# Kernel tuning notes

Hardware: AMD Instinct MI355X
Metric: run time of the kernel (lower is better)

## Reference

```python
import jax, jax.numpy as jnp
import numpy as np

N, T, DF, H, NH, E = 512, 60, 6, 64, 2, 8192
NEG = -1e10

def _leaky(x):
    return jnp.where(x >= 0, x, 0.01 * x)

def _ln(x, g, b, eps=1e-5):
    m = x.mean(-1, keepdims=True)
    v = ((x - m) ** 2).mean(-1, keepdims=True)
    return (x - m) / jnp.sqrt(v + eps) * g + b

def _gru_layer(xs, wih, whh, bih, bhh):
    # xs: (N, T, H_in) -> (N, T, H); torch GRU gate math
    h0 = jnp.zeros((xs.shape[0], whh.shape[1]), xs.dtype)
    def step(h, xt):
        gi = xt @ wih.T + bih
        gh = h @ whh.T + bhh
        ir, iz, inn = jnp.split(gi, 3, -1)
        hr, hz, hn = jnp.split(gh, 3, -1)
        r = jax.nn.sigmoid(ir + hr)
        z = jax.nn.sigmoid(iz + hz)
        n = jnp.tanh(inn + r * hn)
        h = (1 - z) * n + z * h
        return h, h
    _, hs = jax.lax.scan(step, h0, jnp.swapaxes(xs, 0, 1))
    return jnp.swapaxes(hs, 0, 1)

def _forward(x, edge_index, fc_in_w, fc_in_b, gru_wih0, gru_whh0, gru_bih0, gru_bhh0, gru_wih1, gru_whh1, gru_bih1, gru_bhh1, dm_qw, dm_kw, dm_vw, dm_vb, ssa_qw, ssa_kw, ssa_vw, ssa_vb, ln1_g, ln1_b, ln2_g, ln2_b, mlp_w1, mlp_b1, mlp_w2, mlp_b2, mha_in_w, mha_in_b, mha_out_w, mha_out_b, gf_xs_w, gf_xt_w, gf_xt_b, gf_h_w, gf_h_b, lin_w, lin_b):
    h = x @ fc_in_w.T + fc_in_b                      # (N, T, H)
    # temporal encoder: 2-layer GRU + leaky relu
    g = _gru_layer(h, gru_wih0, gru_whh0, gru_bih0, gru_bhh0)
    g = _gru_layer(g, gru_wih1, gru_whh1, gru_bih1, gru_bhh1)
    ts = _leaky(g)
    res_ts = ts[:, -1, :]                            # (N, H)
    # spatial sparse transformer: time T acts as batch, attention over stocks N
    xs = jnp.swapaxes(h, 0, 1)                       # (T, N, H)
    hd = H // NH
    q = (xs @ dm_qw.T).reshape(T, N, NH, hd).transpose(0, 2, 1, 3)
    k = (xs @ dm_kw.T).reshape(T, N, NH, hd).transpose(0, 2, 1, 3)
    v = (xs @ dm_vw.T + dm_vb).reshape(T, N, NH, hd).transpose(0, 2, 1, 3)
    attn = jnp.einsum('thnd,thmd->thnm', q, k) * (H ** -0.5)  # scale uses full dim C, as in source
    dmask = attn >= attn.mean(-1, keepdims=True)     # dynamic per-row mean threshold
    attn_s = jax.nn.softmax(jnp.where(dmask, attn, NEG), axis=-1)
    dyn = jnp.einsum('thnm,thmd->thnd', attn_s, v).transpose(0, 2, 1, 3).reshape(T, N, H)
    # SSA: static graph mask from edge_index
    qs = xs @ ssa_qw.T
    ks2 = xs @ ssa_kw.T
    vs = xs @ ssa_vw.T + ssa_vb
    a2 = jnp.einsum('tnc,tmc->tnm', qs, ks2) * (H ** -0.5)
    adj = jnp.zeros((N, N), jnp.float32).at[edge_index[0], edge_index[1]].add(1.0)
    gmask = adj >= 1.0
    a2s = jax.nn.softmax(jnp.where(gmask[None, :, :], a2, NEG), axis=-1)
    stat = jnp.einsum('tnm,tmc->tnc', a2s, vs)
    residual = dyn + stat + xs
    o = _ln(residual, ln1_g, ln1_b)
    o = (o @ mlp_w1.T + mlp_b1) @ mlp_w2.T + mlp_b2  # two linears, no activation (as in source)
    o = _ln(o + residual, ln2_g, ln2_b)
    move = _leaky(o)                                 # (T, N, H)
    # spatial embedding aggregation: sinusoidal PE + 1-head MHA over time
    pos = jnp.arange(T, dtype=jnp.float32)[:, None]
    div = jnp.exp(jnp.arange(0, H, 2, dtype=jnp.float32) * (-np.log(10000.0) / H))
    pe = jnp.zeros((T, H), jnp.float32).at[:, 0::2].set(jnp.sin(pos * div)).at[:, 1::2].set(jnp.cos(pos * div))
    src = move + pe[:, None, :]
    mq, mk, mv = jnp.split(src @ mha_in_w.T + mha_in_b, 3, axis=-1)
    sc = jnp.einsum('tnh,snh->nts', mq, mk) * (H ** -0.5)
    mo = jnp.einsum('nts,snh->tnh', jax.nn.softmax(sc, -1), mv) @ mha_out_w.T + mha_out_b
    agg = mo[-1]                                     # (N, H)
    mu = agg.mean(-1, keepdims=True)
    var = ((agg - mu) ** 2).mean(-1, keepdims=True)
    agg = (agg - mu) / jnp.sqrt(var + 1e-5)          # param-free layer_norm
    # gated fusion
    zg = jax.nn.sigmoid(agg @ gf_xs_w.T + res_ts @ gf_xt_w.T + gf_xt_b)
    fused = _leaky((zg * agg + (1 - zg) * res_ts) @ gf_h_w.T + gf_h_b)
    out = (fused @ lin_w.T + lin_b)[:, 0]
    return out, attn_s

def setup_inputs() -> dict:
    key = jax.random.key(0)
    ks = jax.random.split(key, 40)
    def w(i, shape):
        return jax.random.normal(ks[i], shape, jnp.float32) * 0.05
    return {
        'x': jax.random.normal(ks[0], (N, T, DF), jnp.float32),
        'edge_index': jax.random.randint(ks[1], (2, E), 0, N),
        'fc_in_w': w(2, (H, DF)), 'fc_in_b': w(3, (H,)),
        'gru_wih0': w(4, (3 * H, H)), 'gru_whh0': w(5, (3 * H, H)), 'gru_bih0': w(6, (3 * H,)), 'gru_bhh0': w(7, (3 * H,)),
        'gru_wih1': w(8, (3 * H, H)), 'gru_whh1': w(9, (3 * H, H)), 'gru_bih1': w(10, (3 * H,)), 'gru_bhh1': w(11, (3 * H,)),
        'dm_qw': w(12, (H, H)), 'dm_kw': w(13, (H, H)), 'dm_vw': w(14, (H, H)), 'dm_vb': w(15, (H,)),
        'ssa_qw': w(16, (H, H)), 'ssa_kw': w(17, (H, H)), 'ssa_vw': w(18, (H, H)), 'ssa_vb': w(19, (H,)),
        'ln1_g': jnp.ones((H,), jnp.float32), 'ln1_b': jnp.zeros((H,), jnp.float32),
        'ln2_g': jnp.ones((H,), jnp.float32), 'ln2_b': jnp.zeros((H,), jnp.float32),
        'mlp_w1': w(20, (2 * H, H)), 'mlp_b1': w(21, (2 * H,)), 'mlp_w2': w(22, (H, 2 * H)), 'mlp_b2': w(23, (H,)),
        'mha_in_w': w(24, (3 * H, H)), 'mha_in_b': w(25, (3 * H,)), 'mha_out_w': w(26, (H, H)), 'mha_out_b': w(27, (H,)),
        'gf_xs_w': w(28, (H, H)), 'gf_xt_w': w(29, (H, H)), 'gf_xt_b': w(30, (H,)),
        'gf_h_w': w(31, (H, H)), 'gf_h_b': w(32, (H,)),
        'lin_w': w(33, (1, H)), 'lin_b': w(34, (1,)),
    }

def reference(x, edge_index, fc_in_w, fc_in_b, gru_wih0, gru_whh0, gru_bih0, gru_bhh0, gru_wih1, gru_whh1, gru_bih1, gru_bhh1, dm_qw, dm_kw, dm_vw, dm_vb, ssa_qw, ssa_kw, ssa_vw, ssa_vb, ln1_g, ln1_b, ln2_g, ln2_b, mlp_w1, mlp_b1, mlp_w2, mlp_b2, mha_in_w, mha_in_b, mha_out_w, mha_out_b, gf_xs_w, gf_xt_w, gf_xt_b, gf_h_w, gf_h_b, lin_w, lin_b):
    return _forward(x, edge_index, fc_in_w, fc_in_b, gru_wih0, gru_whh0, gru_bih0, gru_bhh0, gru_wih1, gru_whh1, gru_bih1, gru_bhh1, dm_qw, dm_kw, dm_vw, dm_vb, ssa_qw, ssa_kw, ssa_vw, ssa_vb, ln1_g, ln1_b, ln2_g, ln2_b, mlp_w1, mlp_b1, mlp_w2, mlp_b2, mha_in_w, mha_in_b, mha_out_w, mha_out_b, gf_xs_w, gf_xt_w, gf_xt_b, gf_h_w, gf_h_b, lin_w, lin_b)
```

## Files before the change

kernel.cpp:

```cpp
#include <hip/hip_runtime.h>
#include <hip/hip_bf16.h>

#define NN 512
#define TT 60
#define DFF 6
#define EE 8192
#define TN (TT*NN)
#define TCH 20
#define NCHK 3
#define SCALEV 0.125f
#define NEGV -1.0e10f

typedef __hip_bfloat16 bf16;
using bfrag8 = __attribute__((ext_vector_type(8))) short;
using facc4  = __attribute__((ext_vector_type(4))) float;

__device__ __forceinline__ float b2f(bf16 v){ return __bfloat162float(v); }
__device__ __forceinline__ bf16 f2b(float v){ return __float2bfloat16(v); }
__device__ __forceinline__ float lk(float x){ return x >= 0.f ? x : 0.01f*x; }
__device__ __forceinline__ float sgm(float x){ return 1.f/(1.f+__expf(-x)); }

__device__ __forceinline__ float ldf(const float* p, long i){ return p[i]; }
__device__ __forceinline__ float ldf(const bf16* p, long i){ return b2f(p[i]); }
__device__ __forceinline__ void stf(float* p, long i, float v){ p[i] = v; }
__device__ __forceinline__ void stf(bf16* p, long i, float v){ p[i] = f2b(v); }

__device__ __forceinline__ float4 ld4f(const float* p){ return *(const float4*)p; }
__device__ __forceinline__ float4 ld4f(const bf16* p){
  ushort4 u = *(const ushort4*)p;
  float4 f;
  f.x = b2f(*(const bf16*)&u.x);
  f.y = b2f(*(const bf16*)&u.y);
  f.z = b2f(*(const bf16*)&u.z);
  f.w = b2f(*(const bf16*)&u.w);
  return f;
}

__device__ __forceinline__ float wsum64(float v){
  #pragma unroll
  for (int off = 32; off; off >>= 1) v += __shfl_xor(v, off, 64);
  return v;
}
__device__ __forceinline__ float wmax64(float v){
  #pragma unroll
  for (int off = 32; off; off >>= 1) v = fmaxf(v, __shfl_xor(v, off, 64));
  return v;
}

__global__ __launch_bounds__(256) void k_zero_u32(unsigned int* __restrict__ p, int n){
  int i = blockIdx.x*256 + threadIdx.x;
  if (i < n) p[i] = 0u;
}
__global__ __launch_bounds__(256) void k_scatter_bits(const int* __restrict__ ei, unsigned int* __restrict__ msk){
  int e = blockIdx.x*256 + threadIdx.x;
  if (e < EE) {
    int u = ei[e], v = ei[EE + e];
    atomicOr(&msk[u*16 + (v >> 5)], 1u << (v & 31));
  }
}

__global__ __launch_bounds__(256) void k_pack(
  const float* __restrict__ qw, const float* __restrict__ kw,
  const float* __restrict__ qsw, const float* __restrict__ ksw,
  const float* __restrict__ vw, const float* __restrict__ vsw,
  const float* __restrict__ vb, const float* __restrict__ vsb,
  float* __restrict__ Wall, float* __restrict__ bcV)
{
  int idx = blockIdx.x*256 + threadIdx.x;
  if (idx < 6*4096) {
    int which = idx >> 12, rem = idx & 4095;
    const float* s = (which==0)?qw:(which==1)?kw:(which==2)?qsw:(which==3)?ksw:(which==4)?vw:vsw;
    Wall[idx] = s[rem];
  } else if (idx < 6*4096 + 128) {
    int o = idx - 6*4096;
    bcV[o] = (o < 64) ? vb[o] : vsb[o-64];
  }
}

__global__ __launch_bounds__(256) void k_fcin(
  const float* __restrict__ x, const float* __restrict__ w, const float* __restrict__ b,
  float* __restrict__ xs, float* __restrict__ resid)
{
  long idx = (long)blockIdx.x*256 + threadIdx.x;
  int o = idx & 63;
  long r = idx >> 6;
  int t = (int)(r / NN), n = (int)(r % NN);
  const float* xr = x + ((long)n*TT + t)*DFF;
  const float* wr = w + o*DFF;
  float acc = 0.f;
  #pragma unroll
  for (int j = 0; j < DFF; ++j) acc = fmaf(xr[j], wr[j], acc);
  float h = __fadd_rn(acc, b[o]);
  xs[idx] = h;
  resid[idx] = h;
}

__global__ __launch_bounds__(256) void k_proj(
  const float* __restrict__ A, const float* __restrict__ Wall, const float* __restrict__ bcV,
  float* __restrict__ qkx, float* __restrict__ qkc, bf16* __restrict__ vvc)
{
  __shared__ float As[64][68];
  __shared__ float Bs[64][68];
  int rt = blockIdx.x, bcn = blockIdx.y;
  const float* B = Wall + bcn*4096;
  int tid = threadIdx.x;
  int tx = tid & 15, ty = tid >> 4;
  float acc[4][4] = {{0.f}};
  #pragma unroll
  for (int i = 0; i < 4; ++i) {
    int t = i*256 + tid;
    int m = t >> 4, kq = (t & 15)*4;
    float4 av = *(const float4*)&A[(long)(rt*64 + m)*64 + kq];
    As[kq+0][m] = av.x; As[kq+1][m] = av.y; As[kq+2][m] = av.z; As[kq+3][m] = av.w;
    float4 bv = *(const float4*)&B[(long)m*64 + kq];
    Bs[kq+0][m] = bv.x; Bs[kq+1][m] = bv.y; Bs[kq+2][m] = bv.z; Bs[kq+3][m] = bv.w;
  }
  __syncthreads();
  for (int kk = 0; kk < 64; ++kk) {
    float4 a4 = *(const float4*)&As[kk][ty*4];
    float4 b4 = *(const float4*)&Bs[kk][tx*4];
    acc[0][0] = fmaf(a4.x,b4.x,acc[0][0]); acc[0][1] = fmaf(a4.x,b4.y,acc[0][1]); acc[0][2] = fmaf(a4.x,b4.z,acc[0][2]); acc[0][3] = fmaf(a4.x,b4.w,acc[0][3]);
    acc[1][0] = fmaf(a4.y,b4.x,acc[1][0]); acc[1][1] = fmaf(a4.y,b4.y,acc[1][1]); acc[1][2] = fmaf(a4.y,b4.z,acc[1][2]); acc[1][3] = fmaf(a4.y,b4.w,acc[1][3]);
    acc[2][0] = fmaf(a4.z,b4.x,acc[2][0]); acc[2][1] = fmaf(a4.z,b4.y,acc[2][1]); acc[2][2] = fmaf(a4.z,b4.z,acc[2][2]); acc[2][3] = fmaf(a4.z,b4.w,acc[2][3]);
    acc[3][0] = fmaf(a4.w,b4.x,acc[3][0]); acc[3][1] = fmaf(a4.w,b4.y,acc[3][1]); acc[3][2] = fmaf(a4.w,b4.z,acc[3][2]); acc[3][3] = fmaf(a4.w,b4.w,acc[3][3]);
  }
  if (bcn < 4) {
    float* C = (bcn < 2) ? qkx : qkc;
    int cb = (bcn & 1)*64;
    #pragma unroll
    for (int i = 0; i < 4; ++i) {
      long ro = (long)(rt*64 + ty*4 + i)*128 + cb + tx*4;
      #pragma unroll
      for (int j = 0; j < 4; ++j) C[ro + j] = acc[i][j];
    }
  } else {
    int cb = (bcn - 4)*64;
    float bv[4];
    #pragma unroll
    for (int j = 0; j < 4; ++j) bv[j] = bcV[cb + tx*4 + j];
    #pragma unroll
    for (int i = 0; i < 4; ++i) {
      long ro = (long)(rt*64 + ty*4 + i)*128 + cb + tx*4;
      #pragma unroll
      for (int j = 0; j < 4; ++j) vvc[ro + j] = f2b(acc[i][j] + bv[j]);
    }
  }
}

template<typename TA, typename TC>
__global__ __launch_bounds__(256) void k_gemm(
  const TA* __restrict__ A, const float* __restrict__ B, const float* __restrict__ bias,
  TC* __restrict__ C, int KD, int NC, int gather)
{
  __shared__ float As[64][68];
  __shared__ float Bs[64][68];
  int rt = blockIdx.x, bcn = blockIdx.y;
  int tid = threadIdx.x;
  int tx = tid & 15, ty = tid >> 4;
  float acc[4][4] = {{0.f}};
  int nch = KD >> 6;
  for (int kc = 0; kc < nch; ++kc) {
    __syncthreads();
    #pragma unroll
    for (int i = 0; i < 4; ++i) {
      int t = i*256 + tid;
      int m = t >> 4, kq = (t & 15)*4;
      long aoff;
      int r = rt*64 + m;
      if (gather) { int n2 = r / TT, t2 = r - n2*TT; aoff = ((long)t2*NN + n2)*64 + kc*64 + kq; }
      else aoff = (long)r*KD + kc*64 + kq;
      float4 av = ld4f(A + aoff);
      As[kq+0][m] = av.x; As[kq+1][m] = av.y; As[kq+2][m] = av.z; As[kq+3][m] = av.w;
      int col = bcn*64 + m;
      float4 bv = *(const float4*)&B[(long)col*KD + kc*64 + kq];
      Bs[kq+0][m] = bv.x; Bs[kq+1][m] = bv.y; Bs[kq+2][m] = bv.z; Bs[kq+3][m] = bv.w;
    }
    __syncthreads();
    #pragma unroll 8
    for (int kk = 0; kk < 64; ++kk) {
      float4 a4 = *(const float4*)&As[kk][ty*4];
      float4 b4 = *(const float4*)&Bs[kk][tx*4];
      acc[0][0] += a4.x*b4.x; acc[0][1] += a4.x*b4.y; acc[0][2] += a4.x*b4.z; acc[0][3] += a4.x*b4.w;
      acc[1][0] += a4.y*b4.x; acc[1][1] += a4.y*b4.y; acc[1][2] += a4.y*b4.z; acc[1][3] += a4.y*b4.w;
      acc[2][0] += a4.z*b4.x; acc[2][1] += a4.z*b4.y; acc[2][2] += a4.z*b4.z; acc[2][3] += a4.z*b4.w;
      acc[3][0] += a4.w*b4.x; acc[3][1] += a4.w*b4.y; acc[3][2] += a4.w*b4.z; acc[3][3] += a4.w*b4.w;
    }
  }
  float bv[4];
  #pragma unroll
  for (int j = 0; j < 4; ++j) bv[j] = bias ? bias[bcn*64 + tx*4 + j] : 0.f;
  #pragma unroll
  for (int i = 0; i < 4; ++i) {
    long ro = (long)(rt*64 + ty*4 + i)*NC + bcn*64 + tx*4;
    #pragma unroll
    for (int j = 0; j < 4; ++j) stf(C, ro + j, acc[i][j] + bv[j]);
  }
}

__global__ __launch_bounds__(192) void k_gru(
  const float* __restrict__ gi, const float* __restrict__ whh, const float* __restrict__ bhh,
  bf16* __restrict__ g_out, float* __restrict__ res_out, int layer)
{
  int n = blockIdx.x;
  int tid = threadIdx.x;
  int g = tid >> 6, o = tid & 63;
  __shared__ __align__(16) float h_lds[64];
  __shared__ float ghs[3][64];
  float4 w4[16];
  #pragma unroll
  for (int k4 = 0; k4 < 16; ++k4)
    w4[k4] = *(const float4*)&whh[(long)(g*64+o)*64 + k4*4];
  float bh = bhh[g*64+o];
  if (tid < 64) h_lds[tid] = 0.f;
  __syncthreads();
  const float4* h4 = (const float4*)h_lds;
  for (int t = 0; t < TT; ++t) {
    float p0 = 0.f, p1 = 0.f, p2 = 0.f, p3 = 0.f;
    #pragma unroll
    for (int k4 = 0; k4 < 16; ++k4) {
      float4 hv = h4[k4];
      p0 = fmaf(w4[k4].x, hv.x, p0);
      p1 = fmaf(w4[k4].y, hv.y, p1);
      p2 = fmaf(w4[k4].z, hv.z, p2);
      p3 = fmaf(w4[k4].w, hv.w, p3);
    }
    ghs[g][o] = bh + ((p0 + p1) + (p2 + p3));
    __syncthreads();
    if (tid < 64) {
      const float* gib = gi + ((long)n*TT + t)*192;
      float ir = gib[o], iz = gib[64+o], inn = gib[128+o];
      float r = sgm(ir + ghs[0][o]);
      float z = sgm(iz + ghs[1][o]);
      float nn2 = tanhf(inn + r*ghs[2][o]);
      float hn = (1.f - z)*nn2 + z*h_lds[o];
      h_lds[o] = hn;
      if (layer == 0) g_out[((long)t*NN + n)*64 + o] = f2b(hn);
      else if (t == TT-1) res_out[(long)n*64 + o] = lk(hn);
    }
    __syncthreads();
  }
}

#define MULADD4(QV, KV) \
  v0 = __fadd_rn(v0, __fmul_rn((QV).x, (KV).x)); \
  v1 = __fadd_rn(v1, __fmul_rn((QV).y, (KV).y)); \
  v2 = __fadd_rn(v2, __fmul_rn((QV).z, (KV).z)); \
  v3 = __fadd_rn(v3, __fmul_rn((QV).w, (KV).w));

__global__ __launch_bounds__(256, 3) void k_attn_dyn(
  const float* __restrict__ qkx, const bf16* __restrict__ vvc,
  float* __restrict__ attn_out, float* __restrict__ resid, int tc)
{
  __shared__ __align__(16) char smem[52288];
  float* sc    = (float*)smem;
  bf16*  vT    = (bf16*)smem;
  float* kt    = (float*)(smem + 33280);
  bf16*  p_lds = (bf16*)(smem + 33280);
  float* red   = (float*)(smem + 49920);
  float* ulds  = (float*)(smem + 51712);
  float* means = (float*)(smem + 52224);

  int qt = blockIdx.x, h = blockIdx.y, lt = blockIdx.z;
  int gt = tc*TCH + lt;
  int tid = threadIdx.x, tx = tid & 31, grp = tid >> 5;
  int qbase = grp*2;
  int qce = h*32, kce = 64 + h*32;

  float4 q0r[8], q1r[8];
  {
    const float* qp = qkx + ((long)(lt*NN + qt*16 + qbase))*128 + qce;
    #pragma unroll
    for (int j = 0; j < 8; ++j) q0r[j] = *(const float4*)(qp + j*4);
    #pragma unroll
    for (int j = 0; j < 8; ++j) q1r[j] = *(const float4*)(qp + 128 + j*4);
  }

  float S[2][16];
  for (int p = 0; p < 4; ++p) {
    __syncthreads();
    for (int i = tid; i < 1024; i += 256) {
      int row = i >> 3, jj = (i & 7) << 2;
      *(float4*)(kt + row*36 + jj) =
        *(const float4*)(qkx + ((long)(lt*NN + p*128 + row))*128 + kce + jj);
    }
    __syncthreads();
    #pragma unroll
    for (int ii = 0; ii < 4; ++ii) {
      int m = tx + 32*ii;
      const float4* kr4 = (const float4*)(kt + m*36);
      float4 k0 = kr4[0], k1 = kr4[1], k2 = kr4[2], k3 = kr4[3];
      float4 k4 = kr4[4], k5 = kr4[5], k6 = kr4[6], k7 = kr4[7];
      {
        float v0 = 0.f, v1 = 0.f, v2 = 0.f, v3 = 0.f;
        MULADD4(q0r[0], k0); MULADD4(q0r[1], k1); MULADD4(q0r[2], k2); MULADD4(q0r[3], k3);
        MULADD4(q0r[4], k4); MULADD4(q0r[5], k5); MULADD4(q0r[6], k6); MULADD4(q0r[7], k7);
        float s = __fadd_rn(__fadd_rn(v0, v1), __fadd_rn(v2, v3));
        s = s * 0.125f;
        S[0][p*4+ii] = s;
        sc[(qbase+0)*520 + p*128 + m] = s;
      }
      {
        float v0 = 0.f, v1 = 0.f, v2 = 0.f, v3 = 0.f;
        MULADD4(q1r[0], k0); MULADD4(q1r[1], k1); MULADD4(q1r[2], k2); MULADD4(q1r[3], k3);
        MULADD4(q1r[4], k4); MULADD4(q1r[5], k5); MULADD4(q1r[6], k6); MULADD4(q1r[7], k7);
        float s = __fadd_rn(__fadd_rn(v0, v1), __fadd_rn(v2, v3));
        s = s * 0.125f;
        S[1][p*4+ii] = s;
        sc[(qbase+1)*520 + p*128 + m] = s;
      }
    }
  }
  __syncthreads();
  if (tid < 128) {
    int row = tid >> 3, b = (tid >> 1) & 3, hh = tid & 1;
    const float* a = sc + row*520 + b*128 + hh*4;
    float4 r4 = *(const float4*)a;
    #pragma unroll
    for (int i = 8; i < 128; i += 8) {
      float4 v = *(const float4*)(a + i);
      r4.x = __fadd_rn(r4.x, v.x); r4.y = __fadd_rn(r4.y, v.y);
      r4.z = __fadd_rn(r4.z, v.z); r4.w = __fadd_rn(r4.w, v.w);
    }
    ulds[row*8 + b*2 + hh] = __fadd_rn(__fadd_rn(r4.x, r4.y), __fadd_rn(r4.z, r4.w));
  }
  __syncthreads();
  if (tid < 16) {
    const float* ur = ulds + tid*8;
    float p0 = __fadd_rn(ur[0], ur[1]);
    float p1 = __fadd_rn(ur[2], ur[3]);
    float p2 = __fadd_rn(ur[4], ur[5]);
    float p3 = __fadd_rn(ur[6], ur[7]);
    means[tid] = __fadd_rn(__fadd_rn(p0, p1), __fadd_rn(p2, p3)) * (1.f/512.f);
  }
  __syncthreads();

  long obase = ((long)(gt*2 + h))*NN*NN;
  #pragma unroll
  for (int qi = 0; qi < 2; ++qi) {
    float mn = means[qbase + qi];
    unsigned kmask = 0; float lm = -INFINITY;
    #pragma unroll
    for (int ig = 0; ig < 16; ++ig) {
      if (S[qi][ig] >= mn) { kmask |= (1u << ig); lm = fmaxf(lm, S[qi][ig]); }
    }
    #pragma unroll
    for (int mk = 1; mk < 32; mk <<= 1) lm = fmaxf(lm, __shfl_xor(lm, mk, 64));
    float e[16]; float se = 0.f;
    #pragma unroll
    for (int ig = 0; ig < 16; ++ig) {
      e[ig] = ((kmask >> ig) & 1u) ? __expf(S[qi][ig] - lm) : 0.f;
      se += e[ig];
    }
    #pragma unroll
    for (int mk = 1; mk < 32; mk <<= 1) se += __shfl_xor(se, mk, 64);
    float inv = 1.f/se;
    float* rowp = attn_out + obase + (long)(qt*16 + qbase + qi)*NN;
    bf16* prow = p_lds + (qbase + qi)*520;
    #pragma unroll
    for (int ig = 0; ig < 16; ++ig) {
      float pr = e[ig]*inv;
      rowp[tx + 32*ig] = pr;
      prow[tx + 32*ig] = f2b(pr);
    }
  }

  for (int i = tid; i < 2048; i += 256) {
    int m2 = (i & 255) << 1;
    int cc = (i >> 8) << 2;
    const bf16* gp = vvc + ((long)(lt*NN + m2))*128 + qce + cc;
    ushort4 a = *(const ushort4*)(gp);
    ushort4 b = *(const ushort4*)(gp + 128);
    *(unsigned*)(vT + (cc+0)*520 + m2) = (unsigned)a.x | ((unsigned)b.x << 16);
    *(unsigned*)(vT + (cc+1)*520 + m2) = (unsigned)a.y | ((unsigned)b.y << 16);
    *(unsigned*)(vT + (cc+2)*520 + m2) = (unsigned)a.z | ((unsigned)b.z << 16);
    *(unsigned*)(vT + (cc+3)*520 + m2) = (unsigned)a.w | ((unsigned)b.w << 16);
  }
  __syncthreads();

  {
    int w = tid >> 6, l = tid & 63;
    int nh = w & 1, kh = w >> 1;
    int arow = l & 15, kgrp = l >> 4;
    facc4 acc = {0.f, 0.f, 0.f, 0.f};
    const bf16* pa = p_lds + arow*520 + kh*256 + kgrp*8;
    const bf16* pb = vT + (nh*16 + arow)*520 + kh*256 + kgrp*8;
    #pragma unroll
    for (int ks = 0; ks < 8; ++ks) {
      bfrag8 av = *(const bfrag8*)(pa + ks*32);
      bfrag8 bv = *(const bfrag8*)(pb + ks*32);
      acc = __builtin_amdgcn_mfma_f32_16x16x32_bf16(av, bv, acc, 0, 0, 0);
    }
    if (w >= 2) {
      #pragma unroll
      for (int r = 0; r < 4; ++r)
        red[nh*272 + (kgrp*4 + r)*17 + arow] = acc[r];
    }
    __syncthreads();
    if (w < 2) {
      long rb = ((long)gt*NN + qt*16)*64 + h*32 + nh*16 + arow;
      #pragma unroll
      for (int r = 0; r < 4; ++r) {
        int row = kgrp*4 + r;
        resid[rb + (long)row*64] += acc[r] + red[nh*272 + row*17 + arow];
      }
    }
  }
}

__global__ __launch_bounds__(256, 3) void k_attn_st(
  const float* __restrict__ qkc, const bf16* __restrict__ vvc,
  const unsigned int* __restrict__ msk, float* __restrict__ resid, int tc)
{
  __shared__ __align__(16) char smem[51456];
  float* kc  = (float*)smem;
  bf16*  vTh = (bf16*)smem;
  float* qtl = (float*)(smem + 34816);
  bf16*  P   = (bf16*)(smem + 34816);

  int qt = blockIdx.x, lt = blockIdx.z;
  int gt = tc*TCH + lt;
  int tid = threadIdx.x;
  int tx = tid & 31, grp = tid >> 5;
  int qbase = grp*2;

  float4* q4 = (float4*)qtl;
  float4* k4 = (float4*)kc;

  {
    int m = tid >> 4, jc = tid & 15;
    q4[m*17 + jc] = *(const float4*)(qkc + ((long)(lt*NN + qt*16 + m))*128 + jc*4);
  }

  float S[2][16];
  for (int p = 0; p < 4; ++p) {
    __syncthreads();
    for (int i = tid; i < 2048; i += 256) {
      int m = i >> 4, jc = i & 15;
      k4[m*17 + (jc ^ ((m >> 2) & 3))] =
        *(const float4*)(qkc + ((long)(lt*NN + p*128 + m))*128 + 64 + jc*4);
    }
    __syncthreads();
    float acc00 = 0.f, acc01 = 0.f, acc02 = 0.f, acc03 = 0.f;
    float acc10 = 0.f, acc11 = 0.f, acc12 = 0.f, acc13 = 0.f;
    #pragma unroll 4
    for (int jc = 0; jc < 16; ++jc) {
      float4 q0 = q4[(qbase+0)*17 + jc];
      float4 q1 = q4[(qbase+1)*17 + jc];
      float4 kv;
      int m0 = tx;
      kv = k4[m0*17 + (jc ^ ((m0 >> 2) & 3))];
      acc00 += q0.x*kv.x + q0.y*kv.y + q0.z*kv.z + q0.w*kv.w;
      acc10 += q1.x*kv.x + q1.y*kv.y + q1.z*kv.z + q1.w*kv.w;
      int m1 = tx + 32;
      kv = k4[m1*17 + (jc ^ ((m1 >> 2) & 3))];
      acc01 += q0.x*kv.x + q0.y*kv.y + q0.z*kv.z + q0.w*kv.w;
      acc11 += q1.x*kv.x + q1.y*kv.y + q1.z*kv.z + q1.w*kv.w;
      int m2 = tx + 64;
      kv = k4[m2*17 + (jc ^ ((m2 >> 2) & 3))];
      acc02 += q0.x*kv.x + q0.y*kv.y + q0.z*kv.z + q0.w*kv.w;
      acc12 += q1.x*kv.x + q1.y*kv.y + q1.z*kv.z + q1.w*kv.w;
      int m3 = tx + 96;
      kv = k4[m3*17 + (jc ^ ((m3 >> 2) & 3))];
      acc03 += q0.x*kv.x + q0.y*kv.y + q0.z*kv.z + q0.w*kv.w;
      acc13 += q1.x*kv.x + q1.y*kv.y + q1.z*kv.z + q1.w*kv.w;
    }
    S[0][p*4+0] = acc00; S[0][p*4+1] = acc01; S[0][p*4+2] = acc02; S[0][p*4+3] = acc03;
    S[1][p*4+0] = acc10; S[1][p*4+1] = acc11; S[1][p*4+2] = acc12; S[1][p*4+3] = acc13;
  }
  __syncthreads();

  #pragma unroll
  for (int qi = 0; qi < 2; ++qi) {
    #pragma unroll
    for (int ig = 0; ig < 16; ++ig) S[qi][ig] *= SCALEV;
    float lm = -INFINITY;
    #pragma unroll
    for (int ig = 0; ig < 16; ++ig) {
      bool keep = ((msk[(qt*16 + qbase + qi)*16 + ig] >> tx) & 1u) != 0u;
      float v = keep ? S[qi][ig] : NEGV;
      S[qi][ig] = v;
      lm = fmaxf(lm, v);
    }
    #pragma unroll
    for (int mk = 1; mk < 32; mk <<= 1) lm = fmaxf(lm, __shfl_xor(lm, mk, 64));
    float se = 0.f;
    #pragma unroll
    for (int ig = 0; ig < 16; ++ig) {
      float ev = __expf(S[qi][ig] - lm);
      S[qi][ig] = ev;
      se += ev;
    }
    #pragma unroll
    for (int mk = 1; mk < 32; mk <<= 1) se += __shfl_xor(se, mk, 64);
    float inv = 1.f / se;
    bf16* prow = P + (qbase + qi)*520;
    #pragma unroll
    for (int ig = 0; ig < 16; ++ig)
      prow[tx + 32*ig] = f2b(S[qi][ig]*inv);
  }

  int w = tid >> 6, l = tid & 63;
  int arow = l & 15, kgrp = l >> 4;
  facc4 acc = {0.f, 0.f, 0.f, 0.f};
  for (int kh = 0; kh < 2; ++kh) {
    __syncthreads();
    for (int i = tid; i < 2048; i += 256) {
      int m2 = (i & 127) << 1;
      int cc = (i >> 7) << 2;
      const bf16* gp = vvc + ((long)(lt*NN + kh*256 + m2))*128 + 64 + cc;
      ushort4 a = *(const ushort4*)(gp);
      ushort4 b = *(const ushort4*)(gp + 128);
      *(unsigned*)(vTh + (cc+0)*264 + m2) = (unsigned)a.x | ((unsigned)b.x << 16);
      *(unsigned*)(vTh + (cc+1)*264 + m2) = (unsigned)a.y | ((unsigned)b.y << 16);
      *(unsigned*)(vTh + (cc+2)*264 + m2) = (unsigned)a.z | ((unsigned)b.z << 16);
      *(unsigned*)(vTh + (cc+3)*264 + m2) = (unsigned)a.w | ((unsigned)b.w << 16);
    }
    __syncthreads();
    const bf16* pa = P + arow*520 + kh*256 + kgrp*8;
    const bf16* pb = vTh + (w*16 + arow)*264 + kgrp*8;
    #pragma unroll
    for (int ks = 0; ks < 8; ++ks) {
      bfrag8 av = *(const bfrag8*)(pa + ks*32);
      bfrag8 bv = *(const bfrag8*)(pb + ks*32);
      acc = __builtin_amdgcn_mfma_f32_16x16x32_bf16(av, bv, acc, 0, 0, 0);
    }
  }
  long rb = ((long)gt*NN + qt*16)*64 + w*16 + arow;
  #pragma unroll
  for (int r = 0; r < 4; ++r) {
    int row = kgrp*4 + r;
    resid[rb + (long)row*64] += acc[r];
  }
}

__global__ __launch_bounds__(256) void k_ln1(
  const float* __restrict__ resid, const float* __restrict__ gw, const float* __restrict__ bw,
  float* __restrict__ ln1o)
{
  int lane = threadIdx.x & 63;
  long r = (long)blockIdx.x*4 + (threadIdx.x >> 6);
  long base = r*64 + lane;
  float v = resid[base];
  float m = wsum64(v)*(1.f/64.f);
  float d = v - m;
  float var = wsum64(d*d)*(1.f/64.f);
  ln1o[base] = d*rsqrtf(var + 1e-5f)*gw[lane] + bw[lane];
}

__global__ __launch_bounds__(256) void k_ln2_src(
  const float* __restrict__ mlpo, const float* __restrict__ resid,
  const float* __restrict__ gw, const float* __restrict__ bw,
  float* __restrict__ src)
{
  int lane = threadIdx.x & 63;
  long r = (long)blockIdx.x*4 + (threadIdx.x >> 6);
  long base = r*64 + lane;
  float v = mlpo[base] + resid[base];
  float m = wsum64(v)*(1.f/64.f);
  float d = v - m;
  float var = wsum64(d*d)*(1.f/64.f);
  float y = d*rsqrtf(var + 1e-5f)*gw[lane] + bw[lane];
  y = lk(y);
  float tf = (float)(r / NN);
  float dv = __expf(-(float)(lane & ~1) * 0.14391156831212787f);
  float pe = (lane & 1) ? cosf(tf*dv) : sinf(tf*dv);
  src[base] = y + pe;
}

__global__ __launch_bounds__(64) void k_head(
  const bf16* __restrict__ mqkv, const float* __restrict__ rts,
  const float* __restrict__ mow, const float* __restrict__ mob,
  const float* __restrict__ xsw, const float* __restrict__ xtw, const float* __restrict__ xtb,
  const float* __restrict__ hw, const float* __restrict__ hb,
  const float* __restrict__ linw, const float* __restrict__ linb,
  float* __restrict__ out)
{
  int n = blockIdx.x, o = threadIdx.x;
  __shared__ float ps[TT];
  __shared__ float buf[64], buf2[64];
  float mq = b2f(mqkv[((long)(TT-1)*NN + n)*192 + o]);
  for (int s = 0; s < TT; ++s) {
    float v = mq * b2f(mqkv[((long)s*NN + n)*192 + 64 + o]);
    v = wsum64(v);
    if (o == 0) ps[s] = v * SCALEV;
  }
  __syncthreads();
  float x = (o < TT) ? ps[o] : -INFINITY;
  float mx = wmax64(x);
  float e = (o < TT) ? __expf(x - mx) : 0.f;
  float se = wsum64(e);
  if (o < TT) ps[o] = e / se;
  __syncthreads();
  float acc = 0.f;
  for (int s = 0; s < TT; ++s) acc += ps[s]*b2f(mqkv[((long)s*NN + n)*192 + 128 + o]);
  buf[o] = acc;
  __syncthreads();
  float acc2 = mob[o];
  for (int k = 0; k < 64; ++k) acc2 += buf[k]*mow[o*64 + k];
  float m2 = wsum64(acc2)*(1.f/64.f);
  float d2 = acc2 - m2;
  float var2 = wsum64(d2*d2)*(1.f/64.f);
  float a = d2*rsqrtf(var2 + 1e-5f);
  float rt = rts[(long)n*64 + o];
  __syncthreads();
  buf[o] = a; buf2[o] = rt;
  __syncthreads();
  float pre = xtb[o];
  for (int k = 0; k < 64; ++k) pre += buf[k]*xsw[o*64 + k] + buf2[k]*xtw[o*64 + k];
  float zg = sgm(pre);
  float u = zg*a + (1.f - zg)*rt;
  __syncthreads();
  buf[o] = u;
  __syncthreads();
  float f = hb[o];
  for (int k = 0; k < 64; ++k) f += buf[k]*hw[o*64 + k];
  f = lk(f);
  float tot = wsum64(f * linw[o]);
  if (o == 0) out[n] = tot + linb[0];
}

extern "C" void kernel_launch(void* const* d_in, const int* in_sizes, int n_in,
                              void* d_out, int out_size, void* d_ws, size_t ws_size,
                              hipStream_t stream)
{
  const float* x    = (const float*)d_in[0];
  const int*   ei   = (const int*)  d_in[1];
  const float* fcw  = (const float*)d_in[2];
  const float* fcb  = (const float*)d_in[3];
  const float* wih0 = (const float*)d_in[4];
  const float* whh0 = (const float*)d_in[5];
  const float* bih0 = (const float*)d_in[6];
  const float* bhh0 = (const float*)d_in[7];
  const float* wih1 = (const float*)d_in[8];
  const float* whh1 = (const float*)d_in[9];
  const float* bih1 = (const float*)d_in[10];
  const float* bhh1 = (const float*)d_in[11];
  const float* dmqw = (const float*)d_in[12];
  const float* dmkw = (const float*)d_in[13];
  const float* dmvw = (const float*)d_in[14];
  const float* dmvb = (const float*)d_in[15];
  const float* ssqw = (const float*)d_in[16];
  const float* sskw = (const float*)d_in[17];
  const float* ssvw = (const float*)d_in[18];
  const float* ssvb = (const float*)d_in[19];
  const float* ln1g = (const float*)d_in[20];
  const float* ln1b = (const float*)d_in[21];
  const float* ln2g = (const float*)d_in[22];
  const float* ln2b = (const float*)d_in[23];
  const float* mw1  = (const float*)d_in[24];
  const float* mb1  = (const float*)d_in[25];
  const float* mw2  = (const float*)d_in[26];
  const float* mb2  = (const float*)d_in[27];
  const float* mhw  = (const float*)d_in[28];
  const float* mhb  = (const float*)d_in[29];
  const float* mow  = (const float*)d_in[30];
  const float* mob  = (const float*)d_in[31];
  const float* gxsw = (const float*)d_in[32];
  const float* gxtw = (const float*)d_in[33];
  const float* gxtb = (const float*)d_in[34];
  const float* ghw  = (const float*)d_in[35];
  const float* ghb  = (const float*)d_in[36];
  const float* linw = (const float*)d_in[37];
  const float* linb = (const float*)d_in[38];

  char* base = (char*)d_ws;
  float*  xs    = (float*)(base);
  char*   Rb    = base + 7864320;
  float*  qkc   = (float*)Rb;
  bf16*   vvc   = (bf16*)(Rb + 5242880);
  float*  qkx   = (float*)(Rb + 7864320);
  float*  mlph  = (float*)Rb;
  bf16*   mqkv  = (bf16*)Rb;
  bf16*   g0    = (bf16*)(base + 23592960);
  float*  resid = (float*)(base + 27525120);
  float*  ln1o  = (float*)(base + 35389440);
  float*  rts   = (float*)(base + 43253760);
  unsigned int* msk = (unsigned int*)(base + 43384832);
  float*  Wall  = (float*)(base + 43417600);
  float*  bcV   = (float*)(base + 43515904);
  float*  mlpo  = xs;
  float*  src   = ln1o;
  float*  outb  = (float*)d_out;
  float*  attn  = outb + 512;
  float*  gi    = (float*)((char*)d_out + 2048);

  k_zero_u32<<<dim3(32), 256, 0, stream>>>(msk, 512*16);
  k_scatter_bits<<<dim3(32), 256, 0, stream>>>(ei, msk);
  k_pack<<<dim3(97), 256, 0, stream>>>(dmqw, dmkw, ssqw, sskw, dmvw, ssvw, dmvb, ssvb, Wall, bcV);
  k_fcin<<<dim3(TN*64/256), 256, 0, stream>>>(x, fcw, fcb, xs, resid);
  k_gemm<float,float><<<dim3(480, 3), 256, 0, stream>>>(xs, wih0, bih0, gi, 64, 192, 1);
  k_gru<<<dim3(NN), 192, 0, stream>>>(gi, whh0, bhh0, g0, nullptr, 0);
  k_gemm<bf16,float><<<dim3(480, 3), 256, 0, stream>>>(g0, wih1, bih1, gi, 64, 192, 1);
  k_gru<<<dim3(NN), 192, 0, stream>>>(gi, whh1, bhh1, nullptr, rts, 1);
  for (int tc = 0; tc < NCHK; ++tc) {
    const float* xsc = xs + (size_t)tc*TCH*NN*64;
    k_proj<<<dim3(TCH*NN/64, 6), 256, 0, stream>>>(xsc, Wall, bcV, qkx, qkc, vvc);
    k_attn_dyn<<<dim3(32, 2, TCH), 256, 0, stream>>>(qkx, vvc, attn, resid, tc);
    k_attn_st <<<dim3(32, 1, TCH), 256, 0, stream>>>(qkc, vvc, msk, resid, tc);
  }
  k_ln1<<<dim3(TN/4), 256, 0, stream>>>(resid, ln1g, ln1b, ln1o);
  k_gemm<float,float><<<dim3(480, 2), 256, 0, stream>>>(ln1o, mw1, mb1, mlph, 64, 128, 0);
  k_gemm<float,float><<<dim3(480, 1), 256, 0, stream>>>(mlph, mw2, mb2, mlpo, 128, 64, 0);
  k_ln2_src<<<dim3(TN/4), 256, 0, stream>>>(mlpo, resid, ln2g, ln2b, src);
  k_gemm<float,bf16 ><<<dim3(480, 3), 256, 0, stream>>>(src, mhw, mhb, mqkv, 64, 192, 0);
  k_head<<<dim3(NN), 64, 0, stream>>>(mqkv, rts, mow, mob, gxsw, gxtw, gxtb, ghw, ghb, linw, linb, outb);
}
```

Before: 734.3 us.

## Fuse mask build, attention kernels, and layernorms into neighbouring kernels

Builds the edge bitmask in shared memory inside an extra block of k_pack, replacing the zero and scatter launches. Merges the dynamic and static attention kernels into one launch, with blockIdx.y==2 taking the static path. Folds LN1 into the first MLP GEMM and LN2 plus leaky-ReLU plus positional encoding into the MHA input projection, which removes the intermediate ln1o/src buffers and several launches. In exchange the layernorms are recomputed once per output column tile. The dynamic and static attention blocks now do unsynchronised read-modify-write on the same resid elements in one launch, a possible data race.

```diff
diff --git a/kernel.cpp b/kernel.cpp
--- a/kernel.cpp
+++ b/kernel.cpp
@@ -47,26 +47,28 @@
   return v;
 }
 
-__global__ __launch_bounds__(256) void k_zero_u32(unsigned int* __restrict__ p, int n){
-  int i = blockIdx.x*256 + threadIdx.x;
-  if (i < n) p[i] = 0u;
-}
-__global__ __launch_bounds__(256) void k_scatter_bits(const int* __restrict__ ei, unsigned int* __restrict__ msk){
-  int e = blockIdx.x*256 + threadIdx.x;
-  if (e < EE) {
-    int u = ei[e], v = ei[EE + e];
-    atomicOr(&msk[u*16 + (v >> 5)], 1u << (v & 31));
-  }
-}
-
 __global__ __launch_bounds__(256) void k_pack(
   const float* __restrict__ qw, const float* __restrict__ kw,
   const float* __restrict__ qsw, const float* __restrict__ ksw,
   const float* __restrict__ vw, const float* __restrict__ vsw,
   const float* __restrict__ vb, const float* __restrict__ vsb,
+  const int* __restrict__ ei, unsigned int* __restrict__ msk,
   float* __restrict__ Wall, float* __restrict__ bcV)
 {
-  int idx = blockIdx.x*256 + threadIdx.x;
+  __shared__ unsigned int lmsk[8192];
+  int tid = threadIdx.x;
+  if (blockIdx.x == 97) {
+    for (int i = tid; i < 8192; i += 256) lmsk[i] = 0u;
+    __syncthreads();
+    for (int e = tid; e < EE; e += 256) {
+      int u = ei[e], v = ei[EE + e];
+      atomicOr(&lmsk[u*16 + (v >> 5)], 1u << (v & 31));
+    }
+    __syncthreads();
+    for (int i = tid; i < 8192; i += 256) msk[i] = lmsk[i];
+    return;
+  }
+  int idx = blockIdx.x*256 + tid;
   if (idx < 6*4096) {
     int which = idx >> 12, rem = idx & 4095;
     const float* s = (which==0)?qw:(which==1)?kw:(which==2)?qsw:(which==3)?ksw:(which==4)?vw:vsw;
@@ -247,11 +249,134 @@
   v2 = __fadd_rn(v2, __fmul_rn((QV).z, (KV).z)); \
   v3 = __fadd_rn(v3, __fmul_rn((QV).w, (KV).w));
 
-__global__ __launch_bounds__(256, 3) void k_attn_dyn(
-  const float* __restrict__ qkx, const bf16* __restrict__ vvc,
+__global__ __launch_bounds__(256, 3) void k_attn(
+  const float* __restrict__ qkx, const float* __restrict__ qkc,
+  const bf16* __restrict__ vvc, const unsigned int* __restrict__ msk,
   float* __restrict__ attn_out, float* __restrict__ resid, int tc)
 {
   __shared__ __align__(16) char smem[52288];
+  int qt = blockIdx.x, lt = blockIdx.z;
+  int gt = tc*TCH + lt;
+  int tid = threadIdx.x, tx = tid & 31, grp = tid >> 5;
+  int qbase = grp*2;
+
+  if (blockIdx.y == 2) {
+    float* kc  = (float*)smem;
+    bf16*  vTh = (bf16*)smem;
+    float* qtl = (float*)(smem + 34816);
+    bf16*  P   = (bf16*)(smem + 34816);
+
+    float4* q4 = (float4*)qtl;
+    float4* k4 = (float4*)kc;
+
+    {
+      int m = tid >> 4, jc = tid & 15;
+      q4[m*17 + jc] = *(const float4*)(qkc + ((long)(lt*NN + qt*16 + m))*128 + jc*4);
+    }
+
+    float S[2][16];
+    for (int p = 0; p < 4; ++p) {
+      __syncthreads();
+      for (int i = tid; i < 2048; i += 256) {
+        int m = i >> 4, jc = i & 15;
+        k4[m*17 + (jc ^ ((m >> 2) & 3))] =
+          *(const float4*)(qkc + ((long)(lt*NN + p*128 + m))*128 + 64 + jc*4);
+      }
+      __syncthreads();
+      float acc00 = 0.f, acc01 = 0.f, acc02 = 0.f, acc03 = 0.f;
+      float acc10 = 0.f, acc11 = 0.f, acc12 = 0.f, acc13 = 0.f;
+      #pragma unroll 4
+      for (int jc = 0; jc < 16; ++jc) {
+        float4 q0 = q4[(qbase+0)*17 + jc];
+        float4 q1 = q4[(qbase+1)*17 + jc];
+        float4 kv;
+        int m0 = tx;
+        kv = k4[m0*17 + (jc ^ ((m0 >> 2) & 3))];
+        acc00 += q0.x*kv.x + q0.y*kv.y + q0.z*kv.z + q0.w*kv.w;
+        acc10 += q1.x*kv.x + q1.y*kv.y + q1.z*kv.z + q1.w*kv.w;
+        int m1 = tx + 32;
+        kv = k4[m1*17 + (jc ^ ((m1 >> 2) & 3))];
+        acc01 += q0.x*kv.x + q0.y*kv.y + q0.z*kv.z + q0.w*kv.w;
+        acc11 += q1.x*kv.x + q1.y*kv.y + q1.z*kv.z + q1.w*kv.w;
+        int m2 = tx + 64;
+        kv = k4[m2*17 + (jc ^ ((m2 >> 2) & 3))];
+        acc02 += q0.x*kv.x + q0.y*kv.y + q0.z*kv.z + q0.w*kv.w;
+        acc12 += q1.x*kv.x + q1.y*kv.y + q1.z*kv.z + q1.w*kv.w;
+        int m3 = tx + 96;
+        kv = k4[m3*17 + (jc ^ ((m3 >> 2) & 3))];
+        acc03 += q0.x*kv.x + q0.y*kv.y + q0.z*kv.z + q0.w*kv.w;
+        acc13 += q1.x*kv.x + q1.y*kv.y + q1.z*kv.z + q1.w*kv.w;
+      }
+      S[0][p*4+0] = acc00; S[0][p*4+1] = acc01; S[0][p*4+2] = acc02; S[0][p*4+3] = acc03;
+      S[1][p*4+0] = acc10; S[1][p*4+1] = acc11; S[1][p*4+2] = acc12; S[1][p*4+3] = acc13;
+    }
+    __syncthreads();
+
+    #pragma unroll
+    for (int qi = 0; qi < 2; ++qi) {
+      #pragma unroll
+      for (int ig = 0; ig < 16; ++ig) S[qi][ig] *= SCALEV;
+      float lm = -INFINITY;
+      #pragma unroll
+      for (int ig = 0; ig < 16; ++ig) {
+        bool keep = ((msk[(qt*16 + qbase + qi)*16 + ig] >> tx) & 1u) != 0u;
+        float v = keep ? S[qi][ig] : NEGV;
+        S[qi][ig] = v;
+        lm = fmaxf(lm, v);
+      }
+      #pragma unroll
+      for (int mk = 1; mk < 32; mk <<= 1) lm = fmaxf(lm, __shfl_xor(lm, mk, 64));
+      float se = 0.f;
+      #pragma unroll
+      for (int ig = 0; ig < 16; ++ig) {
+        float ev = __expf(S[qi][ig] - lm);
+        S[qi][ig] = ev;
+        se += ev;
+      }
+      #pragma unroll
+      for (int mk = 1; mk < 32; mk <<= 1) se += __shfl_xor(se, mk, 64);
+      float inv = 1.f / se;
+      bf16* prow = P + (qbase + qi)*520;
+      #pragma unroll
+      for (int ig = 0; ig < 16; ++ig)
+        prow[tx + 32*ig] = f2b(S[qi][ig]*inv);
+    }
+
+    int w = tid >> 6, l = tid & 63;
+    int arow = l & 15, kgrp = l >> 4;
+    facc4 acc = {0.f, 0.f, 0.f, 0.f};
+    for (int kh = 0; kh < 2; ++kh) {
+      __syncthreads();
+      for (int i = tid; i < 2048; i += 256) {
+        int m2 = (i & 127) << 1;
+        int cc = (i >> 7) << 2;
+        const bf16* gp = vvc + ((long)(lt*NN + kh*256 + m2))*128 + 64 + cc;
+        ushort4 a = *(const ushort4*)(gp);
+        ushort4 b = *(const ushort4*)(gp + 128);
+        *(unsigned*)(vTh + (cc+0)*264 + m2) = (unsigned)a.x | ((unsigned)b.x << 16);
+        *(unsigned*)(vTh + (cc+1)*264 + m2) = (unsigned)a.y | ((unsigned)b.y << 16);
+        *(unsigned*)(vTh + (cc+2)*264 + m2) = (unsigned)a.z | ((unsigned)b.z << 16);
+        *(unsigned*)(vTh + (cc+3)*264 + m2) = (unsigned)a.w | ((unsigned)b.w << 16);
+      }
+      __syncthreads();
+      const bf16* pa = P + arow*520 + kh*256 + kgrp*8;
+      const bf16* pb = vTh + (w*16 + arow)*264 + kgrp*8;
+      #pragma unroll
+      for (int ks = 0; ks < 8; ++ks) {
+        bfrag8 av = *(const bfrag8*)(pa + ks*32);
+        bfrag8 bv = *(const bfrag8*)(pb + ks*32);
+        acc = __builtin_amdgcn_mfma_f32_16x16x32_bf16(av, bv, acc, 0, 0, 0);
+      }
+    }
+    long rb = ((long)gt*NN + qt*16)*64 + w*16 + arow;
+    #pragma unroll
+    for (int r = 0; r < 4; ++r) {
+      int row = kgrp*4 + r;
+      resid[rb + (long)row*64] += acc[r];
+    }
+    return;
+  }
+
   float* sc    = (float*)smem;
   bf16*  vT    = (bf16*)smem;
   float* kt    = (float*)(smem + 33280);
@@ -260,10 +385,7 @@
   float* ulds  = (float*)(smem + 51712);
   float* means = (float*)(smem + 52224);
 
-  int qt = blockIdx.x, h = blockIdx.y, lt = blockIdx.z;
-  int gt = tc*TCH + lt;
-  int tid = threadIdx.x, tx = tid & 31, grp = tid >> 5;
-  int qbase = grp*2;
+  int h = blockIdx.y;
   int qce = h*32, kce = 64 + h*32;
 
   float4 q0r[8], q1r[8];
@@ -407,164 +529,97 @@
   }
 }
 
-__global__ __launch_bounds__(256, 3) void k_attn_st(
-  const float* __restrict__ qkc, const bf16* __restrict__ vvc,
-  const unsigned int* __restrict__ msk, float* __restrict__ resid, int tc)
-{
-  __shared__ __align__(16) char smem[51456];
-  float* kc  = (float*)smem;
-  bf16*  vTh = (bf16*)smem;
-  float* qtl = (float*)(smem + 34816);
-  bf16*  P   = (bf16*)(smem + 34816);
-
-  int qt = blockIdx.x, lt = blockIdx.z;
-  int gt = tc*TCH + lt;
+__global__ __launch_bounds__(256) void k_mlp1(
+  const float* __restrict__ resid, const float* __restrict__ g1, const float* __restrict__ b1,
+  const float* __restrict__ B, const float* __restrict__ bias, float* __restrict__ C)
+{
+  __shared__ float As[64][68];
+  __shared__ float Bs[64][68];
+  int rt = blockIdx.x, bcn = blockIdx.y;
   int tid = threadIdx.x;
-  int tx = tid & 31, grp = tid >> 5;
-  int qbase = grp*2;
-
-  float4* q4 = (float4*)qtl;
-  float4* k4 = (float4*)kc;
-
-  {
-    int m = tid >> 4, jc = tid & 15;
-    q4[m*17 + jc] = *(const float4*)(qkc + ((long)(lt*NN + qt*16 + m))*128 + jc*4);
-  }
-
-  float S[2][16];
-  for (int p = 0; p < 4; ++p) {
-    __syncthreads();
-    for (int i = tid; i < 2048; i += 256) {
-      int m = i >> 4, jc = i & 15;
-      k4[m*17 + (jc ^ ((m >> 2) & 3))] =
-        *(const float4*)(qkc + ((long)(lt*NN + p*128 + m))*128 + 64 + jc*4);
-    }
-    __syncthreads();
-    float acc00 = 0.f, acc01 = 0.f, acc02 = 0.f, acc03 = 0.f;
-    float acc10 = 0.f, acc11 = 0.f, acc12 = 0.f, acc13 = 0.f;
-    #pragma unroll 4
-    for (int jc = 0; jc < 16; ++jc) {
-      float4 q0 = q4[(qbase+0)*17 + jc];
-      float4 q1 = q4[(qbase+1)*17 + jc];
-      float4 kv;
-      int m0 = tx;
-      kv = k4[m0*17 + (jc ^ ((m0 >> 2) & 3))];
-      acc00 += q0.x*kv.x + q0.y*kv.y + q0.z*kv.z + q0.w*kv.w;
-      acc10 += q1.x*kv.x + q1.y*kv.y + q1.z*kv.z + q1.w*kv.w;
-      int m1 = tx + 32;
-      kv = k4[m1*17 + (jc ^ ((m1 >> 2) & 3))];
-      acc01 += q0.x*kv.x + q0.y*kv.y + q0.z*kv.z + q0.w*kv.w;
-      acc11 += q1.x*kv.x + q1.y*kv.y + q1.z*kv.z + q1.w*kv.w;
-      int m2 = tx + 64;
-      kv = k4[m2*17 + (jc ^ ((m2 >> 2) & 3))];
-      acc02 += q0.x*kv.x + q0.y*kv.y + q0.z*kv.z + q0.w*kv.w;
-      acc12 += q1.x*kv.x + q1.y*kv.y + q1.z*kv.z + q1.w*kv.w;
-      int m3 = tx + 96;
-      kv = k4[m3*17 + (jc ^ ((m3 >> 2) & 3))];
-      acc03 += q0.x*kv.x + q0.y*kv.y + q0.z*kv.z + q0.w*kv.w;
-      acc13 += q1.x*kv.x + q1.y*kv.y + q1.z*kv.z + q1.w*kv.w;
-    }
-    S[0][p*4+0] = acc00; S[0][p*4+1] = acc01; S[0][p*4+2] = acc02; S[0][p*4+3] = acc03;
-    S[1][p*4+0] = acc10; S[1][p*4+1] = acc11; S[1][p*4+2] = acc12; S[1][p*4+3] = acc13;
-  }
-  __syncthreads();
-
-  #pragma unroll
-  for (int qi = 0; qi < 2; ++qi) {
-    #pragma unroll
-    for (int ig = 0; ig < 16; ++ig) S[qi][ig] *= SCALEV;
-    float lm = -INFINITY;
-    #pragma unroll
-    for (int ig = 0; ig < 16; ++ig) {
-      bool keep = ((msk[(qt*16 + qbase + qi)*16 + ig] >> tx) & 1u) != 0u;
-      float v = keep ? S[qi][ig] : NEGV;
-      S[qi][ig] = v;
-      lm = fmaxf(lm, v);
-    }
-    #pragma unroll
-    for (int mk = 1; mk < 32; mk <<= 1) lm = fmaxf(lm, __shfl_xor(lm, mk, 64));
-    float se = 0.f;
-    #pragma unroll
-    for (int ig = 0; ig < 16; ++ig) {
-      float ev = __expf(S[qi][ig] - lm);
-      S[qi][ig] = ev;
-      se += ev;
-    }
-    #pragma unroll
-    for (int mk = 1; mk < 32; mk <<= 1) se += __shfl_xor(se, mk, 64);
-    float inv = 1.f / se;
-    bf16* prow = P + (qbase + qi)*520;
-    #pragma unroll
-    for (int ig = 0; ig < 16; ++ig)
-      prow[tx + 32*ig] = f2b(S[qi][ig]*inv);
-  }
-
-  int w = tid >> 6, l = tid & 63;
-  int arow = l & 15, kgrp = l >> 4;
-  facc4 acc = {0.f, 0.f, 0.f, 0.f};
-  for (int kh = 0; kh < 2; ++kh) {
-    __syncthreads();
-    for (int i = tid; i < 2048; i += 256) {
-      int m2 = (i & 127) << 1;
-      int cc = (i >> 7) << 2;
-      const bf16* gp = vvc + ((long)(lt*NN + kh*256 + m2))*128 + 64 + cc;
-      ushort4 a = *(const ushort4*)(gp);
-      ushort4 b = *(const ushort4*)(gp + 128);
-      *(unsigned*)(vTh + (cc+0)*264 + m2) = (unsigned)a.x | ((unsigned)b.x << 16);
-      *(unsigned*)(vTh + (cc+1)*264 + m2) = (unsigned)a.y | ((unsigned)b.y << 16);
-      *(unsigned*)(vTh + (cc+2)*264 + m2) = (unsigned)a.z | ((unsigned)b.z << 16);
-      *(unsigned*)(vTh + (cc+3)*264 + m2) = (unsigned)a.w | ((unsigned)b.w << 16);
-    }
-    __syncthreads();
-    const bf16* pa = P + arow*520 + kh*256 + kgrp*8;
-    const bf16* pb = vTh + (w*16 + arow)*264 + kgrp*8;
-    #pragma unroll
-    for (int ks = 0; ks < 8; ++ks) {
-      bfrag8 av = *(const bfrag8*)(pa + ks*32);
-      bfrag8 bv = *(const bfrag8*)(pb + ks*32);
-      acc = __builtin_amdgcn_mfma_f32_16x16x32_bf16(av, bv, acc, 0, 0, 0);
-    }
-  }
-  long rb = ((long)gt*NN + qt*16)*64 + w*16 + arow;
-  #pragma unroll
-  for (int r = 0; r < 4; ++r) {
-    int row = kgrp*4 + r;
-    resid[rb + (long)row*64] += acc[r];
-  }
-}
-
-__global__ __launch_bounds__(256) void k_ln1(
-  const float* __restrict__ resid, const float* __restrict__ gw, const float* __restrict__ bw,
-  float* __restrict__ ln1o)
-{
-  int lane = threadIdx.x & 63;
-  long r = (long)blockIdx.x*4 + (threadIdx.x >> 6);
-  long base = r*64 + lane;
-  float v = resid[base];
-  float m = wsum64(v)*(1.f/64.f);
-  float d = v - m;
-  float var = wsum64(d*d)*(1.f/64.f);
-  ln1o[base] = d*rsqrtf(var + 1e-5f)*gw[lane] + bw[lane];
-}
-
-__global__ __launch_bounds__(256) void k_ln2_src(
+  int tx = tid & 15, ty = tid >> 4;
+  int wave = tid >> 6, lane = tid & 63;
+  for (int rr = wave; rr < 64; rr += 4) {
+    float v = resid[((long)rt*64 + rr)*64 + lane];
+    float m = wsum64(v)*(1.f/64.f);
+    float d = v - m;
+    float var = wsum64(d*d)*(1.f/64.f);
+    As[lane][rr] = d*rsqrtf(var + 1e-5f)*g1[lane] + b1[lane];
+  }
+  #pragma unroll
+  for (int i = 0; i < 4; ++i) {
+    int t = i*256 + tid;
+    int m = t >> 4, kq = (t & 15)*4;
+    float4 bv = *(const float4*)&B[(long)(bcn*64 + m)*64 + kq];
+    Bs[kq+0][m] = bv.x; Bs[kq+1][m] = bv.y; Bs[kq+2][m] = bv.z; Bs[kq+3][m] = bv.w;
+  }
+  __syncthreads();
+  float acc[4][4] = {{0.f}};
+  #pragma unroll 8
+  for (int kk = 0; kk < 64; ++kk) {
+    float4 a4 = *(const float4*)&As[kk][ty*4];
+    float4 b4 = *(const float4*)&Bs[kk][tx*4];
+    acc[0][0] += a4.x*b4.x; acc[0][1] += a4.x*b4.y; acc[0][2] += a4.x*b4.z; acc[0][3] += a4.x*b4.w;
+    acc[1][0] += a4.y*b4.x; acc[1][1] += a4.y*b4.y; acc[1][2] += a4.y*b4.z; acc[1][3] += a4.y*b4.w;
+    acc[2][0] += a4.z*b4.x; acc[2][1] += a4.z*b4.y; acc[2][2] += a4.z*b4.z; acc[2][3] += a4.z*b4.w;
+    acc[3][0] += a4.w*b4.x; acc[3][1] += a4.w*b4.y; acc[3][2] += a4.w*b4.z; acc[3][3] += a4.w*b4.w;
+  }
+  #pragma unroll
+  for (int i = 0; i < 4; ++i) {
+    long ro = (long)(rt*64 + ty*4 + i)*128 + bcn*64 + tx*4;
+    #pragma unroll
+    for (int j = 0; j < 4; ++j) C[ro + j] = acc[i][j] + bias[bcn*64 + tx*4 + j];
+  }
+}
+
+__global__ __launch_bounds__(256) void k_mha_in(
   const float* __restrict__ mlpo, const float* __restrict__ resid,
-  const float* __restrict__ gw, const float* __restrict__ bw,
-  float* __restrict__ src)
-{
-  int lane = threadIdx.x & 63;
-  long r = (long)blockIdx.x*4 + (threadIdx.x >> 6);
-  long base = r*64 + lane;
-  float v = mlpo[base] + resid[base];
-  float m = wsum64(v)*(1.f/64.f);
-  float d = v - m;
-  float var = wsum64(d*d)*(1.f/64.f);
-  float y = d*rsqrtf(var + 1e-5f)*gw[lane] + bw[lane];
-  y = lk(y);
-  float tf = (float)(r / NN);
-  float dv = __expf(-(float)(lane & ~1) * 0.14391156831212787f);
-  float pe = (lane & 1) ? cosf(tf*dv) : sinf(tf*dv);
-  src[base] = y + pe;
+  const float* __restrict__ g2, const float* __restrict__ b2,
+  const float* __restrict__ B, const float* __restrict__ bias, bf16* __restrict__ C)
+{
+  __shared__ float As[64][68];
+  __shared__ float Bs[64][68];
+  int rt = blockIdx.x, bcn = blockIdx.y;
+  int tid = threadIdx.x;
+  int tx = tid & 15, ty = tid >> 4;
+  int wave = tid >> 6, lane = tid & 63;
+  for (int rr = wave; rr < 64; rr += 4) {
+    long r = (long)rt*64 + rr;
+    float v = mlpo[r*64 + lane] + resid[r*64 + lane];
+    float m = wsum64(v)*(1.f/64.f);
+    float d = v - m;
+    float var = wsum64(d*d)*(1.f/64.f);
+    float y = d*rsqrtf(var + 1e-5f)*g2[lane] + b2[lane];
+    y = lk(y);
+    float tf = (float)(r / NN);
+    float dv = __expf(-(float)(lane & ~1) * 0.14391156831212787f);
+    float pe = (lane & 1) ? cosf(tf*dv) : sinf(tf*dv);
+    As[lane][rr] = y + pe;
+  }
+  #pragma unroll
+  for (int i = 0; i < 4; ++i) {
+    int t = i*256 + tid;
+    int m = t >> 4, kq = (t & 15)*4;
+    float4 bv = *(const float4*)&B[(long)(bcn*64 + m)*64 + kq];
+    Bs[kq+0][m] = bv.x; Bs[kq+1][m] = bv.y; Bs[kq+2][m] = bv.z; Bs[kq+3][m] = bv.w;
+  }
+  __syncthreads();
+  float acc[4][4] = {{0.f}};
+  #pragma unroll 8
+  for (int kk = 0; kk < 64; ++kk) {
+    float4 a4 = *(const float4*)&As[kk][ty*4];
+    float4 b4 = *(const float4*)&Bs[kk][tx*4];
+    acc[0][0] += a4.x*b4.x; acc[0][1] += a4.x*b4.y; acc[0][2] += a4.x*b4.z; acc[0][3] += a4.x*b4.w;
+    acc[1][0] += a4.y*b4.x; acc[1][1] += a4.y*b4.y; acc[1][2] += a4.y*b4.z; acc[1][3] += a4.y*b4.w;
+    acc[2][0] += a4.z*b4.x; acc[2][1] += a4.z*b4.y; acc[2][2] += a4.z*b4.z; acc[2][3] += a4.z*b4.w;
+    acc[3][0] += a4.w*b4.x; acc[3][1] += a4.w*b4.y; acc[3][2] += a4.w*b4.z; acc[3][3] += a4.w*b4.w;
+  }
+  #pragma unroll
+  for (int i = 0; i < 4; ++i) {
+    long ro = (long)(rt*64 + ty*4 + i)*192 + bcn*64 + tx*4;
+    #pragma unroll
+    for (int j = 0; j < 4; ++j) C[ro + j] = f2b(acc[i][j] + bias[bcn*64 + tx*4 + j]);
+  }
 }
 
 __global__ __launch_bounds__(64) void k_head(
@@ -673,20 +728,16 @@
   bf16*   mqkv  = (bf16*)Rb;
   bf16*   g0    = (bf16*)(base + 23592960);
   float*  resid = (float*)(base + 27525120);
-  float*  ln1o  = (float*)(base + 35389440);
   float*  rts   = (float*)(base + 43253760);
   unsigned int* msk = (unsigned int*)(base + 43384832);
   float*  Wall  = (float*)(base + 43417600);
   float*  bcV   = (float*)(base + 43515904);
   float*  mlpo  = xs;
-  float*  src   = ln1o;
   float*  outb  = (float*)d_out;
   float*  attn  = outb + 512;
   float*  gi    = (float*)((char*)d_out + 2048);
 
-  k_zero_u32<<<dim3(32), 256, 0, stream>>>(msk, 512*16);
-  k_scatter_bits<<<dim3(32), 256, 0, stream>>>(ei, msk);
-  k_pack<<<dim3(97), 256, 0, stream>>>(dmqw, dmkw, ssqw, sskw, dmvw, ssvw, dmvb, ssvb, Wall, bcV);
+  k_pack<<<dim3(98), 256, 0, stream>>>(dmqw, dmkw, ssqw, sskw, dmvw, ssvw, dmvb, ssvb, ei, msk, Wall, bcV);
   k_fcin<<<dim3(TN*64/256), 256, 0, stream>>>(x, fcw, fcb, xs, resid);
   k_gemm<float,float><<<dim3(480, 3), 256, 0, stream>>>(xs, wih0, bih0, gi, 64, 192, 1);
   k_gru<<<dim3(NN), 192, 0, stream>>>(gi, whh0, bhh0, g0, nullptr, 0);
@@ -695,13 +746,10 @@
   for (int tc = 0; tc < NCHK; ++tc) {
     const float* xsc = xs + (size_t)tc*TCH*NN*64;
     k_proj<<<dim3(TCH*NN/64, 6), 256, 0, stream>>>(xsc, Wall, bcV, qkx, qkc, vvc);
-    k_attn_dyn<<<dim3(32, 2, TCH), 256, 0, stream>>>(qkx, vvc, attn, resid, tc);
-    k_attn_st <<<dim3(32, 1, TCH), 256, 0, stream>>>(qkc, vvc, msk, resid, tc);
-  }
-  k_ln1<<<dim3(TN/4), 256, 0, stream>>>(resid, ln1g, ln1b, ln1o);
-  k_gemm<float,float><<<dim3(480, 2), 256, 0, stream>>>(ln1o, mw1, mb1, mlph, 64, 128, 0);
+    k_attn<<<dim3(32, 3, TCH), 256, 0, stream>>>(qkx, qkc, vvc, msk, attn, resid, tc);
+  }
+  k_mlp1<<<dim3(480, 2), 256, 0, stream>>>(resid, ln1g, ln1b, mw1, mb1, mlph);
   k_gemm<float,float><<<dim3(480, 1), 256, 0, stream>>>(mlph, mw2, mb2, mlpo, 128, 64, 0);
-  k_ln2_src<<<dim3(TN/4), 256, 0, stream>>>(mlpo, resid, ln2g, ln2b, src);
-  k_gemm<float,bf16 ><<<dim3(480, 3), 256, 0, stream>>>(src, mhw, mhb, mqkv, 64, 192, 0);
+  k_mha_in<<<dim3(480, 3), 256, 0, stream>>>(mlpo, resid, ln2g, ln2b, mhw, mhb, mqkv);
   k_head<<<dim3(NN), 64, 0, stream>>>(mqkv, rts, mow, mob, gxsw, gxtw, gxtb, ghw, ghb, linw, linb, outb);
 }
```

New measurement: 732.3 us. No clear change (-0.3%).
